# Kernel tuning notes

Measured on AMD Instinct MI355X. Metric: run time of the kernel, lower is better.

Reference implementation:

```python
import jax, jax.numpy as jnp
import numpy as np

N, C, L, K = 8, 128, 1024, 100   # batch, channels, encoded seq len, num_negatives
TEMP = 0.5                        # contrastive temperature
EPS = 1e-8                        # cosine-similarity norm clamp (torch default)


def setup_inputs() -> dict:
    key = jax.random.key(0)
    kz, kc, kn = jax.random.split(key, 3)
    z = jax.random.normal(kz, (N, C, L), dtype=jnp.float32)
    c = jax.random.normal(kc, (N, C, L + 1), dtype=jnp.float32)
    # Uniform sampling of K distinct indices per (n, l), excluding l itself:
    # equivalent to torch.multinomial(ones(L,L)-eye(L), K) per row, per sample.
    noise = jax.random.uniform(kn, (N, L, L), dtype=jnp.float32)
    noise = noise - 2.0 * jnp.eye(L, dtype=jnp.float32)  # push self-index below everything
    _, neg_inds = jax.lax.top_k(noise, K)                # (N, L, K) int32, distinct, != l
    return {"z": z, "c": c, "neg_inds": neg_inds.astype(jnp.int32)}


def reference(z, c, neg_inds):
    # z: (N, C, L) unmasked convencoder features; c: (N, C, L+1) transformer out
    n, ch, l = z.shape
    z_seq = jnp.transpose(z, (0, 2, 1))                  # (N, L, C)
    # gather negatives: (N, L, K, C)
    negatives = z_seq[jnp.arange(n)[:, None, None], neg_inds]
    # drop start token, move to (N, L, 1, C)
    c_seq = jnp.transpose(c[..., 1:], (0, 2, 1))[:, :, None, :]
    z_tgt = z_seq[:, :, None, :]                         # (N, L, 1, C)
    targets = jnp.concatenate([z_tgt, negatives], axis=2)  # (N, L, K+1, C)
    # cosine similarity along C with torch-style eps clamping
    dot = jnp.sum(c_seq * targets, axis=-1)              # (N, L, K+1)
    c_norm = jnp.maximum(jnp.sqrt(jnp.sum(c_seq * c_seq, axis=-1)), EPS)
    t_norm = jnp.maximum(jnp.sqrt(jnp.sum(targets * targets, axis=-1)), EPS)
    logits = dot / (c_norm * t_norm) / TEMP              # (N, L, K+1)
    # mask negatives that exactly equal the context vector
    neg_in_tgt = jnp.all(c_seq == negatives, axis=-1)    # (N, L, K)
    neg_logits = jnp.where(neg_in_tgt, -jnp.inf, logits[:, :, 1:])
    logits = jnp.concatenate([logits[:, :, :1], neg_logits], axis=2)
    return logits.reshape(-1, K + 1)                     # (N*L, K+1)
```

## Files before the change

### kernel.cpp

```cpp
#include <hip/hip_runtime.h>
#include <math.h>

#define N 8
#define C 128
#define L 1024
#define K 100
#define TEMP 0.5f
#define EPS 1e-8f
#define NT (N * L)
#define ROWS 32

typedef _Float16 half8 __attribute__((ext_vector_type(8)));
typedef float f32x4 __attribute__((ext_vector_type(4)));


__global__ void __launch_bounds__(512)
transpose_frag(const float* __restrict__ z, const float* __restrict__ c,
               half8* __restrict__ zf, half8* __restrict__ cf,
               float* __restrict__ zp, float* __restrict__ cp) {
    __shared__ float tile[64][65];
    __shared__ float part[8][64];
    const int d = blockIdx.x;
    const int n = d & 7;
    const int rest = d >> 3;
    const int which = rest & 1;
    const int c0 = ((rest >> 1) & 1) * 64;
    const int l0 = (rest >> 2) * 64;
    const float* src = which ? c : z;
    half8* dst = which ? cf : zf;
    float* pdst = which ? cp : zp;
    const int slen = which ? (L + 1) : L;
    const int off = which;
    const int tx = threadIdx.x;
    const int ty = threadIdx.y;
#pragma unroll
    for (int i = 0; i < 8; i++) {
        int chn = c0 + ty + i * 8;
        tile[ty + i * 8][tx] = src[((size_t)(n * C + chn)) * slen + off + l0 + tx];
    }
    __syncthreads();
    float p = 0.f;
    half8 hv;
#pragma unroll
    for (int q = 0; q < 8; q++) {
        float v = tile[ty * 8 + q][tx];
        p += v * v;
        hv[q] = (_Float16)v;
    }
    const int l = l0 + tx;
    const int ch = c0 + ty * 8;
    const int ks = ch >> 5, kg = (ch >> 3) & 3;
    dst[(((size_t)(n * 64 + (l >> 4)) * 4 + ks) << 6) + (l & 15) + (kg << 4)] = hv;
    part[ty][tx] = p;
    __syncthreads();
    if (ty == 0) {
        float sm = 0.f;
#pragma unroll
        for (int i = 0; i < 8; i++) sm += part[i][tx];
        pdst[(((size_t)n << 10) + l0 + tx) * 2 + (c0 >> 6)] = sm;
    }
}

__global__ void __launch_bounds__(512, 2)
gemm_gather(const half8* __restrict__ zf, const half8* __restrict__ cf,
            const int* __restrict__ neg_inds,
            const float* __restrict__ zp, const float* __restrict__ cp,
            const float* __restrict__ z_orig, const float* __restrict__ c_orig,
            float* __restrict__ out) {
    __shared__ _Float16 dotH[ROWS * L];
    __shared__ float ztn[L];
    __shared__ float ztr[L];
    __shared__ int   nil[ROWS * K];
    __shared__ float outF[ROWS * (K + 1)];
    const int tid  = threadIdx.x;
    const int lane = tid & 63;
    const int w    = tid >> 6;
    const int n    = blockIdx.x & 7;
    const int tA   = blockIdx.x >> 3;
    const int ntg0 = (n << 10) + (tA << 5);

    const float2* zp2 = (const float2*)zp + ((size_t)n << 10);
    for (int i = tid; i < L; i += 512) {
        float2 tv = zp2[i];
        float tn = tv.x + tv.y;
        ztn[i] = tn;
        ztr[i] = rsqrtf(fmaxf(tn, EPS * EPS));
    }
    const int* nb = neg_inds + (size_t)ntg0 * K;
    for (int i = tid; i < ROWS * K; i += 512) nil[i] = nb[i];

    const size_t nbase = (size_t)n << 14;
    half8 a[2][4];
#pragma unroll
    for (int at = 0; at < 2; at++)
#pragma unroll
        for (int ks = 0; ks < 4; ks++)
            a[at][ks] = cf[nbase + ((((tA << 1) + at) * 4 + ks) << 6) + lane];

    f32x4 acc[2][8];
#pragma unroll
    for (int at = 0; at < 2; at++)
#pragma unroll
        for (int i = 0; i < 8; i++)
#pragma unroll
            for (int r = 0; r < 4; r++) acc[at][i][r] = 0.f;

#pragma unroll
    for (int ks = 0; ks < 4; ks++) {
        half8 b[8];
#pragma unroll
        for (int nt = 0; nt < 8; nt++)
            b[nt] = zf[nbase + ((size_t)(((w << 3) + nt) * 4 + ks) << 6) + lane];
#pragma unroll
        for (int nt = 0; nt < 8; nt++)
            acc[0][nt] = __builtin_amdgcn_mfma_f32_16x16x32_f16(a[0][ks], b[nt], acc[0][nt], 0, 0, 0);
#pragma unroll
        for (int nt = 0; nt < 8; nt++)
            acc[1][nt] = __builtin_amdgcn_mfma_f32_16x16x32_f16(a[1][ks], b[nt], acc[1][nt], 0, 0, 0);
    }

    const int r16 = lane & 15;
    const int kg  = lane >> 4;
#pragma unroll
    for (int at = 0; at < 2; at++)
#pragma unroll
        for (int nt = 0; nt < 8; nt++)
#pragma unroll
            for (int r = 0; r < 4; r++) {
                const int row = (at << 4) + (kg << 2) + r;
                const int col = (w << 7) + (nt << 4) + r16;
                dotH[row * L + (col ^ (kg << 4))] = (_Float16)acc[at][nt][r];
            }
    __syncthreads();

    const int row = tid >> 4;
    const int sub = tid & 15;
    const int t   = (tA << 5) + row;
    const int ksw = ((row >> 2) & 3) << 4;
    const float2 cpv = ((const float2*)cp)[ntg0 + row];
    const float cn = cpv.x + cpv.y;
    const float rs_c = 2.0f * rsqrtf(fmaxf(cn, EPS * EPS));

#pragma unroll
    for (int j = 0; j < 7; j++) {
        const int kk = sub * 7 + j;
        if (kk <= K) {
            const int col = (kk == 0) ? t : nil[row * K + kk - 1];
            const float dot = (float)dotH[row * L + (col ^ ksw)];
            const float tn = ztn[col];
            float logit = dot * rs_c * ztr[col];
            if (kk > 0) {
                const float ds = cn - 2.f * dot + tn;
                if (ds < 0.05f * cn) {
                    bool eq = true;
                    for (int q = 0; q < C; q++) {
                        float cv = c_orig[((size_t)(n * C + q)) * (L + 1) + t + 1];
                        float zv = z_orig[((size_t)(n * C + q)) * L + col];
                        eq = eq && (cv == zv);
                    }
                    if (eq) logit = -INFINITY;
                }
            }
            outF[row * (K + 1) + kk] = logit;
        }
    }
    __syncthreads();

    float* ob = out + (size_t)ntg0 * (K + 1);
    for (int i = tid; i < ROWS * (K + 1); i += 512) ob[i] = outF[i];
}

extern "C" void kernel_launch(void* const* d_in, const int* in_sizes, int n_in,
                              void* d_out, int out_size, void* d_ws, size_t ws_size,
                              hipStream_t stream) {
    const float* z   = (const float*)d_in[0];
    const float* c   = (const float*)d_in[1];
    const int*   neg = (const int*)d_in[2];
    float* out = (float*)d_out;

    half8* zf = (half8*)d_ws;
    half8* cf = zf + (size_t)N * 16384;
    float* zp = (float*)(cf + (size_t)N * 16384);
    float* cp = zp + (size_t)NT * 2;

    transpose_frag<<<dim3(512), dim3(64, 8), 0, stream>>>(z, c, zf, cf, zp, cp);
    gemm_gather<<<dim3(N * (L / ROWS)), 512, 0, stream>>>(zf, cf, neg, zp, cp, z, c, out);
}
```

Measured before the change: 73.81 us.

## Fuse context transpose and norm into gemm kernel, transpose only z upfront

The c tensor is no longer transposed and converted to fp16 fragments in the preprocessing kernel. Each gemm block now loads its 32-row slice of c directly into shared memory (aliasing the dotH buffer), builds the MFMA A fragments from there and computes the context norms with a shuffle reduction. This halves the preprocessing grid and drops a workspace round trip for c. In exchange it adds an extra sync plus strided global reads of c inside the main kernel, and it lowers the launch bound's minimum blocks per CU from 2 to 1, which may raise register use and cut occupancy.

```diff
diff --git a/kernel.cpp b/kernel.cpp
--- a/kernel.cpp
+++ b/kernel.cpp
@@ -14,29 +14,23 @@
 typedef float f32x4 __attribute__((ext_vector_type(4)));
 
 
+
 __global__ void __launch_bounds__(512)
-transpose_frag(const float* __restrict__ z, const float* __restrict__ c,
-               half8* __restrict__ zf, half8* __restrict__ cf,
-               float* __restrict__ zp, float* __restrict__ cp) {
+transpose_z(const float* __restrict__ z, half8* __restrict__ zf,
+            float* __restrict__ zp) {
     __shared__ float tile[64][65];
     __shared__ float part[8][64];
     const int d = blockIdx.x;
     const int n = d & 7;
     const int rest = d >> 3;
-    const int which = rest & 1;
-    const int c0 = ((rest >> 1) & 1) * 64;
-    const int l0 = (rest >> 2) * 64;
-    const float* src = which ? c : z;
-    half8* dst = which ? cf : zf;
-    float* pdst = which ? cp : zp;
-    const int slen = which ? (L + 1) : L;
-    const int off = which;
+    const int c0 = (rest & 1) * 64;
+    const int l0 = (rest >> 1) * 64;
     const int tx = threadIdx.x;
     const int ty = threadIdx.y;
 #pragma unroll
     for (int i = 0; i < 8; i++) {
         int chn = c0 + ty + i * 8;
-        tile[ty + i * 8][tx] = src[((size_t)(n * C + chn)) * slen + off + l0 + tx];
+        tile[ty + i * 8][tx] = z[((size_t)(n * C + chn)) * L + l0 + tx];
     }
     __syncthreads();
     float p = 0.f;
@@ -50,21 +44,20 @@
     const int l = l0 + tx;
     const int ch = c0 + ty * 8;
     const int ks = ch >> 5, kg = (ch >> 3) & 3;
-    dst[(((size_t)(n * 64 + (l >> 4)) * 4 + ks) << 6) + (l & 15) + (kg << 4)] = hv;
+    zf[(((size_t)(n * 64 + (l >> 4)) * 4 + ks) << 6) + (l & 15) + (kg << 4)] = hv;
     part[ty][tx] = p;
     __syncthreads();
     if (ty == 0) {
         float sm = 0.f;
 #pragma unroll
         for (int i = 0; i < 8; i++) sm += part[i][tx];
-        pdst[(((size_t)n << 10) + l0 + tx) * 2 + (c0 >> 6)] = sm;
+        zp[(((size_t)n << 10) + l0 + tx) * 2 + (c0 >> 6)] = sm;
     }
 }
 
-__global__ void __launch_bounds__(512, 2)
-gemm_gather(const half8* __restrict__ zf, const half8* __restrict__ cf,
-            const int* __restrict__ neg_inds,
-            const float* __restrict__ zp, const float* __restrict__ cp,
+__global__ void __launch_bounds__(512, 1)
+gemm_gather(const half8* __restrict__ zf, const int* __restrict__ neg_inds,
+            const float* __restrict__ zp,
             const float* __restrict__ z_orig, const float* __restrict__ c_orig,
             float* __restrict__ out) {
     __shared__ _Float16 dotH[ROWS * L];
@@ -72,12 +65,16 @@
     __shared__ float ztr[L];
     __shared__ int   nil[ROWS * K];
     __shared__ float outF[ROWS * (K + 1)];
+    __shared__ float cnL[ROWS];
+    float* ct = (float*)dotH;
+
     const int tid  = threadIdx.x;
     const int lane = tid & 63;
     const int w    = tid >> 6;
     const int n    = blockIdx.x & 7;
     const int tA   = blockIdx.x >> 3;
-    const int ntg0 = (n << 10) + (tA << 5);
+    const int t0   = tA << 5;
+    const int ntg0 = (n << 10) + t0;
 
     const float2* zp2 = (const float2*)zp + ((size_t)n << 10);
     for (int i = tid; i < L; i += 512) {
@@ -89,14 +86,40 @@
     const int* nb = neg_inds + (size_t)ntg0 * K;
     for (int i = tid; i < ROWS * K; i += 512) nil[i] = nb[i];
 
+    {
+        const int ch = tid >> 2;
+        const int j0 = (tid & 3) * 8;
+        const float* cr = c_orig + ((size_t)(n * C + ch)) * (L + 1) + t0 + 1 + j0;
+#pragma unroll
+        for (int jj = 0; jj < 8; jj++) ct[ch * 33 + j0 + jj] = cr[jj];
+    }
+    __syncthreads();
+
+    const int r16 = lane & 15;
+    const int kg  = lane >> 4;
+    half8 a[2][4];
+#pragma unroll
+    for (int at = 0; at < 2; at++)
+#pragma unroll
+        for (int ks = 0; ks < 4; ks++)
+#pragma unroll
+            for (int e = 0; e < 8; e++)
+                a[at][ks][e] = (_Float16)ct[(ks * 32 + kg * 8 + e) * 33 + (at << 4) + r16];
+    {
+        const int row = tid >> 4, sub = tid & 15;
+        float cs = 0.f;
+#pragma unroll
+        for (int i = 0; i < 8; i++) {
+            float v = ct[(sub * 8 + i) * 33 + row];
+            cs += v * v;
+        }
+        cs += __shfl_xor(cs, 1); cs += __shfl_xor(cs, 2);
+        cs += __shfl_xor(cs, 4); cs += __shfl_xor(cs, 8);
+        if (sub == 0) cnL[row] = cs;
+    }
+    __syncthreads();
+
     const size_t nbase = (size_t)n << 14;
-    half8 a[2][4];
-#pragma unroll
-    for (int at = 0; at < 2; at++)
-#pragma unroll
-        for (int ks = 0; ks < 4; ks++)
-            a[at][ks] = cf[nbase + ((((tA << 1) + at) * 4 + ks) << 6) + lane];
-
     f32x4 acc[2][8];
 #pragma unroll
     for (int at = 0; at < 2; at++)
@@ -119,8 +142,6 @@
             acc[1][nt] = __builtin_amdgcn_mfma_f32_16x16x32_f16(a[1][ks], b[nt], acc[1][nt], 0, 0, 0);
     }
 
-    const int r16 = lane & 15;
-    const int kg  = lane >> 4;
 #pragma unroll
     for (int at = 0; at < 2; at++)
 #pragma unroll
@@ -135,10 +156,9 @@
 
     const int row = tid >> 4;
     const int sub = tid & 15;
-    const int t   = (tA << 5) + row;
+    const int t   = t0 + row;
     const int ksw = ((row >> 2) & 3) << 4;
-    const float2 cpv = ((const float2*)cp)[ntg0 + row];
-    const float cn = cpv.x + cpv.y;
+    const float cn = cnL[row];
     const float rs_c = 2.0f * rsqrtf(fmaxf(cn, EPS * EPS));
 
 #pragma unroll
@@ -179,10 +199,8 @@
     float* out = (float*)d_out;
 
     half8* zf = (half8*)d_ws;
-    half8* cf = zf + (size_t)N * 16384;
-    float* zp = (float*)(cf + (size_t)N * 16384);
-    float* cp = zp + (size_t)NT * 2;
-
-    transpose_frag<<<dim3(512), dim3(64, 8), 0, stream>>>(z, c, zf, cf, zp, cp);
-    gemm_gather<<<dim3(N * (L / ROWS)), 512, 0, stream>>>(zf, cf, neg, zp, cp, z, c, out);
+    float* zp = (float*)(zf + (size_t)N * 16384);
+
+    transpose_z<<<dim3(256), dim3(64, 8), 0, stream>>>(z, zf, zp);
+    gemm_gather<<<dim3(N * (L / ROWS)), 512, 0, stream>>>(zf, neg, zp, z, c, out);
 }
```

After: 74.37 us. No clear change (+0.8%).
